# Kernel tuning notes

Measured on AMD Instinct MI355X. Metric: run time of the kernel, lower is better.

## Reference

```python
import jax, jax.numpy as jnp
import numpy as np
from jax import lax

A_SCALES = np.array([8., 16., 32.])
A_RATIOS = np.array([0.5, 1., 2.])
STRIDE = 16
PRE_NMS = 6000
POST_NMS = 300
NMS_THRESH = 0.7
MIN_SIZE = 16.0
NEG = -1e9


def _gen_anchors(base_size=16):
    w = h = float(base_size)
    x = y = 0.5 * (base_size - 1)
    size = w * h
    ws = np.round(np.sqrt(size / A_RATIOS))
    hs = np.round(ws * A_RATIOS)
    out = []
    for wi, hi in zip(ws, hs):
        WS = wi * A_SCALES
        HS = hi * A_SCALES
        out.append(np.stack([x - 0.5 * (WS - 1), y - 0.5 * (HS - 1),
                             x + 0.5 * (WS - 1), y + 0.5 * (HS - 1)], 1))
    return np.concatenate(out, 0).astype(np.float32)  # [9,4]

ANCHORS = _gen_anchors()


def _conv(x, w, b, pad):
    y = lax.conv_general_dilated(x, w, (1, 1), [(pad, pad), (pad, pad)],
                                 dimension_numbers=('NCHW', 'OIHW', 'NCHW'))
    return y + b[None, :, None, None]


def _nms(boxes, scores):
    # fixed-size greedy NMS: POST_NMS iterations of argmax + suppress
    areas = (boxes[:, 2] - boxes[:, 0] + 1.) * (boxes[:, 3] - boxes[:, 1] + 1.)
    def step(s, _):
        i = jnp.argmax(s)
        b = boxes[i]
        ix1 = jnp.maximum(b[0], boxes[:, 0]); iy1 = jnp.maximum(b[1], boxes[:, 1])
        ix2 = jnp.minimum(b[2], boxes[:, 2]); iy2 = jnp.minimum(b[3], boxes[:, 3])
        inter = jnp.maximum(ix2 - ix1 + 1., 0.) * jnp.maximum(iy2 - iy1 + 1., 0.)
        iou = inter / (areas[i] + areas - inter)
        return jnp.where(iou > NMS_THRESH, NEG, s), i
    _, keep = lax.scan(step, scores, None, length=POST_NMS)
    return keep


def reference(base_feat, img_info, gt_boxes, W1, b1, Wc, bc, Wb, bb):
    A = ANCHORS.shape[0]  # 9
    h = jax.nn.relu(_conv(base_feat, W1, b1, 1))          # [1,512,H,W]
    scores = _conv(h, Wc, bc, 0)                           # [1,2A,H,W]
    deltas = _conv(h, Wb, bb, 0)                           # [1,4A,H,W]
    H, W = scores.shape[2], scores.shape[3]
    # reshape(2) -> softmax over dim1 -> reshape back (RPN.reshape trick)
    probs = jax.nn.softmax(scores.reshape(1, 2, A * H, W), axis=1).reshape(1, 2 * A, H, W)
    fg = jnp.transpose(probs[0, A:], (1, 2, 0)).reshape(-1)      # [H*W*A], (h,w,a) order
    d = jnp.transpose(deltas[0], (1, 2, 0)).reshape(-1, 4)       # [H*W*A,4]
    sx, sy = jnp.meshgrid(jnp.arange(W, dtype=jnp.float32) * STRIDE,
                          jnp.arange(H, dtype=jnp.float32) * STRIDE)
    shifts = jnp.stack([sx, sy, sx, sy], -1).reshape(-1, 4)      # [H*W,4]
    anch = (shifts[:, None, :] + jnp.asarray(ANCHORS)[None, :, :]).reshape(-1, 4)
    # bbox_transform_inv
    wdt = anch[:, 2] - anch[:, 0] + 1.
    hgt = anch[:, 3] - anch[:, 1] + 1.
    cx = anch[:, 0] + 0.5 * wdt
    cy = anch[:, 1] + 0.5 * hgt
    pcx = d[:, 0] * wdt + cx
    pcy = d[:, 1] * hgt + cy
    pw = jnp.exp(d[:, 2]) * wdt
    ph = jnp.exp(d[:, 3]) * hgt
    x1 = jnp.clip(pcx - 0.5 * pw, 0., img_info[1] - 1.)
    y1 = jnp.clip(pcy - 0.5 * ph, 0., img_info[0] - 1.)
    x2 = jnp.clip(pcx + 0.5 * pw, 0., img_info[1] - 1.)
    y2 = jnp.clip(pcy + 0.5 * ph, 0., img_info[0] - 1.)
    props = jnp.stack([x1, y1, x2, y2], 1)
    ms = MIN_SIZE * img_info[2]
    valid = ((x2 - x1 + 1.) >= ms) & ((y2 - y1 + 1.) >= ms)
    sc = jnp.where(valid, fg, NEG)
    top_sc, top_idx = lax.top_k(sc, PRE_NMS)
    top_boxes = props[top_idx]
    keep = _nms(top_boxes, top_sc)
    out = top_boxes[keep]                                  # [POST_NMS,4]
    return jnp.concatenate([jnp.zeros((POST_NMS, 1), out.dtype), out], 1)


def setup_inputs() -> dict:
    key = jax.random.key(0)
    ks = jax.random.split(key, 6)
    H, W, C = 64, 96, 1024
    base_feat = jax.random.normal(ks[0], (1, C, H, W), jnp.float32)
    img_info = jnp.array([H * 16., W * 16., 1.], jnp.float32)
    gt_boxes = jax.random.uniform(ks[1], (8, 6), jnp.float32) * 100.0
    W1 = jax.random.normal(ks[2], (512, C, 3, 3), jnp.float32) * np.float32(np.sqrt(2.0 / (C * 9)))
    b1 = jnp.zeros((512,), jnp.float32)
    Wc = jax.random.normal(ks[3], (18, 512, 1, 1), jnp.float32) * np.float32(1.0 / np.sqrt(512))
    bc = jnp.zeros((18,), jnp.float32)
    Wb = jax.random.normal(ks[4], (36, 512, 1, 1), jnp.float32) * np.float32(0.01 / np.sqrt(512))
    bb = jnp.zeros((36,), jnp.float32)
    return {"base_feat": base_feat, "img_info": img_info, "gt_boxes": gt_boxes,
            "W1": W1, "b1": b1, "Wc": Wc, "bc": bc, "Wb": Wb, "bb": bb}
```

## Files before the change

### kernel.cpp

```cpp
#include <hip/hip_runtime.h>
#include <math.h>

#define HH 64
#define WW 96
#define NPX (HH*WW)
#define CIN 1024
#define CMID 512
#define NA 9
#define NANCH (NPX*NA)
#define PRE_NMS 6000
#define POST_NMS 300
#define NEGV -1e9f
#define NBINS 16384
#define BUFCAP 8192
#define MASKW 94

#define PYS 66
#define PXS 98
#define NCB 32
#define SCL 2048.0f
#define INV_SCL (1.0f/2048.0f)

#define K2_CS 16
#define K2_CC (CMID/K2_CS)

typedef _Float16 f16x8 __attribute__((ext_vector_type(8)));
typedef float f32x4 __attribute__((ext_vector_type(4)));

__constant__ float c_anch[9][4] = {
    {-84.f, -40.f,  99.f,  55.f},
    {-176.f,-88.f, 191.f, 103.f},
    {-360.f,-184.f,375.f, 199.f},
    {-56.f, -56.f,  71.f,  71.f},
    {-120.f,-120.f,135.f, 135.f},
    {-248.f,-248.f,263.f, 263.f},
    {-36.f, -80.f,  51.f,  95.f},
    {-80.f,-168.f,  95.f, 183.f},
    {-168.f,-344.f,183.f, 359.f}
};

__device__ __forceinline__ unsigned int fkey(float f) {
    unsigned int b = __float_as_uint(f);
    return (b & 0x80000000u) ? ~b : (b | 0x80000000u);
}
__device__ __forceinline__ float fkey_inv(unsigned int k) {
    unsigned int b = (k & 0x80000000u) ? (k & 0x7fffffffu) : ~k;
    return __uint_as_float(b);
}
__device__ __forceinline__ int score_bin(float s) {
    if (!(s > 0.f)) return 0;
    int b = (int)(s * (float)NBINS);
    return b > NBINS - 1 ? NBINS - 1 : b;
}

__global__ __launch_bounds__(256) void prep_x(const float* __restrict__ x,
                                              _Float16* __restrict__ xh,
                                              _Float16* __restrict__ xl) {
    __shared__ float t[64][65];
    int tid = threadIdx.x;
    int c0 = blockIdx.x * 64;
    int p0 = blockIdx.y * 64;
    int g = tid >> 6, l = tid & 63;
#pragma unroll
    for (int k = 0; k < 16; k++) {
        int cl = g * 16 + k;
        t[cl][l] = x[(size_t)(c0 + cl) * NPX + p0 + l];
    }
    __syncthreads();
#pragma unroll
    for (int k = 0; k < 16; k++) {
        int pl = g * 16 + k;
        int p = p0 + pl;
        int y = p / WW, xc = p - y * WW;
        int c = c0 + l;
        float v = t[l][pl];
        _Float16 hv = (_Float16)v;
        _Float16 lv = (_Float16)((v - (float)hv) * SCL);
        size_t o = (((size_t)(c >> 5) * PYS + (y + 1)) * PXS + (xc + 1)) * 32 + (c & 31);
        xh[o] = hv;
        xl[o] = lv;
    }
}

__global__ __launch_bounds__(256) void prep_w(const float* __restrict__ w,
                                              _Float16* __restrict__ wh,
                                              _Float16* __restrict__ wl) {
    __shared__ _Float16 sh[CIN * 9];
    __shared__ _Float16 sl[CIN * 9];
    int tid = threadIdx.x;
    int oc = blockIdx.x;
    for (int i = tid; i < CIN * 9; i += 256) {
        float v = w[(size_t)oc * CIN * 9 + i];
        _Float16 hv = (_Float16)v;
        sh[i] = hv;
        sl[i] = (_Float16)((v - (float)hv) * SCL);
    }
    __syncthreads();
    for (int i = tid; i < CIN * 9; i += 256) {
        int tap = i >> 10;
        int c = i & 1023;
        size_t o = (((size_t)tap * NCB + (c >> 5)) * CMID + oc) * 32 + (c & 31);
        wh[o] = sh[c * 9 + tap];
        wl[o] = sl[c * 9 + tap];
    }
}

__global__ __launch_bounds__(256, 2) void conv3_mfma(const _Float16* __restrict__ xh,
                                                     const _Float16* __restrict__ xl,
                                                     const _Float16* __restrict__ wh,
                                                     const _Float16* __restrict__ wl,
                                                     const float* __restrict__ b1,
                                                     float* __restrict__ h) {
    __shared__ float4 red[4][2][64];
    int tid = threadIdx.x;
    int lane = tid & 63;
    int wv = tid >> 6;
    int sp = blockIdx.x;
    int ty0 = (sp / 6) * 4;
    int tx0 = (sp % 6) * 16;
    int oc0 = blockIdx.y * 32;

    int la = lane & 15;
    int kg = lane >> 4;

    f32x4 acch[4][2], accc[4][2];
#pragma unroll
    for (int m = 0; m < 4; m++)
#pragma unroll
        for (int n = 0; n < 2; n++) {
            acch[m][n] = (f32x4){0.f, 0.f, 0.f, 0.f};
            accc[m][n] = (f32x4){0.f, 0.f, 0.f, 0.f};
        }

    int cb0 = wv * (NCB / 4);
    for (int cbi = 0; cbi < NCB / 4; cbi++) {
        int cb = cb0 + cbi;
#pragma unroll
        for (int tap = 0; tap < 9; tap++) {
            const int ky = tap / 3, kx = tap % 3;
            f16x8 ah[4], al[4];
#pragma unroll
            for (int m = 0; m < 4; m++) {
                int aoff = ((cb * PYS + (ty0 + m + ky)) * PXS + (tx0 + kx + la)) * 32 + kg * 8;
                ah[m] = *(const f16x8*)(xh + aoff);
                al[m] = *(const f16x8*)(xl + aoff);
            }
#pragma unroll
            for (int n = 0; n < 2; n++) {
                int boff = ((tap * NCB + cb) * CMID + oc0 + n * 16 + la) * 32 + kg * 8;
                f16x8 bh = *(const f16x8*)(wh + boff);
                f16x8 bl = *(const f16x8*)(wl + boff);
#pragma unroll
                for (int m = 0; m < 4; m++) {
                    acch[m][n] = __builtin_amdgcn_mfma_f32_16x16x32_f16(ah[m], bh, acch[m][n], 0, 0, 0);
                    accc[m][n] = __builtin_amdgcn_mfma_f32_16x16x32_f16(al[m], bh, accc[m][n], 0, 0, 0);
                    accc[m][n] = __builtin_amdgcn_mfma_f32_16x16x32_f16(ah[m], bl, accc[m][n], 0, 0, 0);
                }
            }
        }
    }

#pragma unroll
    for (int m = 0; m < 4; m++) {
        __syncthreads();
#pragma unroll
        for (int n = 0; n < 2; n++) {
            f32x4 t = acch[m][n];
            f32x4 c = accc[m][n];
            float4 w4;
            w4.x = t[0] + c[0] * INV_SCL;
            w4.y = t[1] + c[1] * INV_SCL;
            w4.z = t[2] + c[2] * INV_SCL;
            w4.w = t[3] + c[3] * INV_SCL;
            red[wv][n][lane] = w4;
        }
        __syncthreads();
        if (tid < 128) {
            int n = tid >> 6, l = tid & 63;
            float4 s0 = red[0][n][l], s1 = red[1][n][l];
            float4 s2 = red[2][n][l], s3 = red[3][n][l];
            int oc = oc0 + n * 16 + (l & 15);
            float bs = b1[oc];
            float4 s;
            s.x = fmaxf(s0.x + s1.x + s2.x + s3.x + bs, 0.f);
            s.y = fmaxf(s0.y + s1.y + s2.y + s3.y + bs, 0.f);
            s.z = fmaxf(s0.z + s1.z + s2.z + s3.z + bs, 0.f);
            s.w = fmaxf(s0.w + s1.w + s2.w + s3.w + bs, 0.f);
            int y = ty0 + m;
            int px0 = tx0 + (l >> 4) * 4;
            *(float4*)&h[(size_t)oc * NPX + y * WW + px0] = s;
        }
    }
}

__global__ __launch_bounds__(256) void conv1x1_part(const float* __restrict__ h,
                                                    const float* __restrict__ wc,
                                                    const float* __restrict__ wb,
                                                    float* __restrict__ psum) {
    __shared__ float wT[K2_CC][56];
    int tid = threadIdx.x;
    int px = blockIdx.x * 256 + tid;
    int g = blockIdx.y;
    int cb = g * K2_CC;
    for (int i = tid; i < K2_CC * 54; i += 256) {
        int c = i / 54, o = i - c * 54;
        float wv = (o < 18) ? wc[o * CMID + cb + c] : wb[(o - 18) * CMID + cb + c];
        wT[c][o] = wv;
    }
    __syncthreads();
    float acc[54];
#pragma unroll
    for (int o = 0; o < 54; o++) acc[o] = 0.f;
    for (int c = 0; c < K2_CC; c++) {
        float hv = h[(size_t)(cb + c) * NPX + px];
#pragma unroll
        for (int o = 0; o < 54; o++) acc[o] += wT[c][o] * hv;
    }
    for (int o = 0; o < 54; o++)
        psum[((size_t)g * 54 + o) * NPX + px] = acc[o];
}

__global__ __launch_bounds__(256) void conv1x1_reduce(const float* __restrict__ psum,
                                                      const float* __restrict__ bc,
                                                      const float* __restrict__ bb,
                                                      float* __restrict__ sd) {
    int i = blockIdx.x * 256 + threadIdx.x;
    if (i >= 54 * NPX) return;
    int o = i / NPX;
    float s = (o < 18) ? bc[o] : bb[o - 18];
    for (int g = 0; g < K2_CS; g++) s += psum[(size_t)g * 54 * NPX + i];
    sd[i] = s;
}

__global__ __launch_bounds__(256) void proposals_k(const float* __restrict__ sd,
                                                   const float* __restrict__ info,
                                                   float* __restrict__ props,
                                                   float* __restrict__ scv,
                                                   unsigned int* __restrict__ hist) {
    int i = blockIdx.x * 256 + threadIdx.x;
    if (i >= NANCH) return;
    int a = i % NA;
    int p = i / NA;
    int hy = p / WW, wx = p - hy * WW;

    float s0 = sd[a * NPX + p], s1 = sd[(a + NA) * NPX + p];
    float m = fmaxf(s0, s1);
    float e0 = expf(s0 - m), e1 = expf(s1 - m);
    float fg = e1 / (e0 + e1);

    float d0 = sd[(18 + 4 * a + 0) * NPX + p];
    float d1 = sd[(18 + 4 * a + 1) * NPX + p];
    float d2 = sd[(18 + 4 * a + 2) * NPX + p];
    float d3 = sd[(18 + 4 * a + 3) * NPX + p];

    float sx = wx * 16.f, sy = hy * 16.f;
    float ax1 = c_anch[a][0] + sx, ay1 = c_anch[a][1] + sy;
    float ax2 = c_anch[a][2] + sx, ay2 = c_anch[a][3] + sy;
    float wdt = ax2 - ax1 + 1.f;
    float hgt = ay2 - ay1 + 1.f;
    float cx = ax1 + 0.5f * wdt;
    float cy = ay1 + 0.5f * hgt;
    float pcx = d0 * wdt + cx;
    float pcy = d1 * hgt + cy;
    float pw = expf(d2) * wdt;
    float ph = expf(d3) * hgt;

    float imh = info[0], imw = info[1], iscale = info[2];
    float x1 = fminf(fmaxf(pcx - 0.5f * pw, 0.f), imw - 1.f);
    float y1 = fminf(fmaxf(pcy - 0.5f * ph, 0.f), imh - 1.f);
    float x2 = fminf(fmaxf(pcx + 0.5f * pw, 0.f), imw - 1.f);
    float y2 = fminf(fmaxf(pcy + 0.5f * ph, 0.f), imh - 1.f);

    float ms = 16.f * iscale;
    bool valid = ((x2 - x1 + 1.f) >= ms) && ((y2 - y1 + 1.f) >= ms);
    float s = valid ? fg : NEGV;

    props[(size_t)i * 4 + 0] = x1;
    props[(size_t)i * 4 + 1] = y1;
    props[(size_t)i * 4 + 2] = x2;
    props[(size_t)i * 4 + 3] = y2;
    scv[i] = s;
    atomicAdd(&hist[score_bin(s)], 1u);
}

__global__ __launch_bounds__(1024) void scan_hist(const unsigned int* __restrict__ hist,
                                                  unsigned int* __restrict__ params) {
    __shared__ unsigned int psum[1024];
    int tid = threadIdx.x;
    unsigned int s = 0;
    for (int k = 0; k < 16; k++) s += hist[tid * 16 + k];
    psum[tid] = s;
    __syncthreads();
    if (tid == 0) {
        unsigned int run = 0;
        int B = 0;
        int t;
        for (t = 1023; t >= 0; t--) {
            if (run + psum[t] >= PRE_NMS) break;
            run += psum[t];
        }
        if (t >= 0) {
            unsigned int r2 = run;
            B = t * 16;
            for (int b = t * 16 + 15; b >= t * 16; b--) {
                r2 += hist[b];
                if (r2 >= PRE_NMS) { B = b; break; }
            }
        }
        params[0] = (unsigned int)B;
    }
}

__global__ __launch_bounds__(256) void gather_top(const float* __restrict__ scv,
                                                  const unsigned int* __restrict__ params,
                                                  unsigned long long* __restrict__ buf,
                                                  unsigned int* __restrict__ counter) {
    int i = blockIdx.x * 256 + threadIdx.x;
    if (i >= NANCH) return;
    float s = scv[i];
    if (score_bin(s) >= (int)params[0]) {
        unsigned int pos = atomicAdd(counter, 1u);
        if (pos < BUFCAP) {
            unsigned long long key = ((unsigned long long)fkey(s) << 32) |
                                     (unsigned int)(~(unsigned int)i);
            buf[pos] = key;
        }
    }
}

__global__ __launch_bounds__(1024) void sort_top(unsigned long long* __restrict__ buf,
                                                 const unsigned int* __restrict__ counter,
                                                 const float* __restrict__ props,
                                                 float* __restrict__ top_boxes,
                                                 float* __restrict__ top_sc) {
    __shared__ unsigned long long arr[BUFCAP];
    int tid = threadIdx.x;
    unsigned int m = counter[0];
    if (m > BUFCAP) m = BUFCAP;
    for (int i = tid; i < BUFCAP; i += 1024) arr[i] = (i < (int)m) ? buf[i] : 0ULL;
    __syncthreads();
    for (int k = 2; k <= BUFCAP; k <<= 1) {
        for (int j = k >> 1; j > 0; j >>= 1) {
            for (int i = tid; i < BUFCAP; i += 1024) {
                int l = i ^ j;
                if (l > i) {
                    unsigned long long a = arr[i], b = arr[l];
                    bool dir = ((i & k) == 0);
                    if (dir ? (a < b) : (a > b)) { arr[i] = b; arr[l] = a; }
                }
            }
            __syncthreads();
        }
    }
    for (int t = tid; t < PRE_NMS; t += 1024) {
        unsigned long long v = arr[t];
        unsigned int key = (unsigned int)(v >> 32);
        unsigned int idx = ~((unsigned int)v);
        top_sc[t] = fkey_inv(key);
        float4 bx = *(const float4*)&props[(size_t)idx * 4];
        *(float4*)&top_boxes[(size_t)t * 4] = bx;
    }
}

__global__ __launch_bounds__(256) void iou_mask(const float* __restrict__ top_boxes,
                                                unsigned long long* __restrict__ mask) {
    int wid = (blockIdx.x * 256 + threadIdx.x) >> 6;
    int lane = threadIdx.x & 63;
    if (wid >= PRE_NMS) return;
    float4 b = *(const float4*)&top_boxes[(size_t)wid * 4];
    float ab = (b.z - b.x + 1.f) * (b.w - b.y + 1.f);
    for (int cj = 0; cj < MASKW; cj++) {
        int j = cj * 64 + lane;
        bool sup = false;
        if (j < PRE_NMS) {
            float4 c = *(const float4*)&top_boxes[(size_t)j * 4];
            float ac = (c.z - c.x + 1.f) * (c.w - c.y + 1.f);
            float ix1 = fmaxf(b.x, c.x), iy1 = fmaxf(b.y, c.y);
            float ix2 = fminf(b.z, c.z), iy2 = fminf(b.w, c.w);
            float inter = fmaxf(ix2 - ix1 + 1.f, 0.f) * fmaxf(iy2 - iy1 + 1.f, 0.f);
            float iou = inter / (ab + ac - inter);
            sup = iou > 0.7f;
        }
        unsigned long long m = __ballot(sup);
        if (lane == 0) mask[(size_t)wid * MASKW + cj] = m;
    }
}

__global__ __launch_bounds__(64) void nms_greedy(const float* __restrict__ top_boxes,
                                                 const unsigned long long* __restrict__ mask,
                                                 float* __restrict__ out) {
    int lane = threadIdx.x;
    unsigned long long r0 = 0ULL;
    unsigned long long r1;
    if (lane < 29)      r1 = 0ULL;
    else if (lane == 29) r1 = ~((1ULL << 48) - 1);
    else                r1 = ~0ULL;
    for (int t = 0; t < POST_NMS; t++) {
        unsigned long long w0 = ~r0;
        unsigned long long w1 = ~r1;
        unsigned long long B0 = __ballot(w0 != 0ULL);
        unsigned long long B1 = __ballot(w1 != 0ULL);
        int pos = 0;
        if (B0) {
            int wl = __builtin_ctzll(B0);
            unsigned long long bits = __shfl(w0, wl);
            pos = wl * 64 + __builtin_ctzll(bits);
        } else if (B1) {
            int wl = __builtin_ctzll(B1);
            unsigned long long bits = __shfl(w1, wl);
            pos = (64 + wl) * 64 + __builtin_ctzll(bits);
        }
        if (lane == 0) {
            float4 bb = *(const float4*)&top_boxes[(size_t)pos * 4];
            out[t * 5 + 0] = 0.f;
            out[t * 5 + 1] = bb.x;
            out[t * 5 + 2] = bb.y;
            out[t * 5 + 3] = bb.z;
            out[t * 5 + 4] = bb.w;
        }
        r0 |= mask[(size_t)pos * MASKW + lane];
        if (lane < 30) r1 |= mask[(size_t)pos * MASKW + 64 + lane];
    }
}

extern "C" void kernel_launch(void* const* d_in, const int* in_sizes, int n_in,
                              void* d_out, int out_size, void* d_ws, size_t ws_size,
                              hipStream_t stream) {
    const float* base = (const float*)d_in[0];
    const float* info = (const float*)d_in[1];
    const float* W1 = (const float*)d_in[3];
    const float* b1 = (const float*)d_in[4];
    const float* Wc = (const float*)d_in[5];
    const float* bc = (const float*)d_in[6];
    const float* Wb = (const float*)d_in[7];
    const float* Bb = (const float*)d_in[8];
    float* out = (float*)d_out;
    char* ws = (char*)d_ws;

    const size_t SZ_XT = (size_t)PYS * PXS * CIN * 2;
    const size_t SZ_WT = (size_t)9 * CMID * CIN * 2;
    const size_t OFF_XH = 0;
    const size_t OFF_XL = OFF_XH + SZ_XT;
    const size_t OFF_WH = OFF_XL + SZ_XT;
    const size_t OFF_WL = OFF_WH + SZ_WT;
    const size_t OFF_H  = OFF_WL + SZ_WT;
    const size_t OFF_SD   = OFF_H + (size_t)CMID * NPX * 4;
    const size_t OFF_PROPS= OFF_SD + (size_t)54 * NPX * 4;
    const size_t OFF_SCV  = OFF_PROPS + (size_t)NANCH * 16;
    const size_t OFF_HIST = OFF_SCV + (size_t)NANCH * 4;
    const size_t OFF_PAR  = OFF_HIST + (size_t)NBINS * 4;
    const size_t OFF_BUF  = OFF_PAR + 256;
    const size_t OFF_TB   = OFF_BUF + (size_t)BUFCAP * 8;
    const size_t OFF_TS   = OFF_TB + (size_t)PRE_NMS * 16;
    const size_t OFF_PSUM = OFF_XH;
    const size_t OFF_MASK = OFF_XH;

    _Float16* xh = (_Float16*)(ws + OFF_XH);
    _Float16* xl = (_Float16*)(ws + OFF_XL);
    _Float16* wh = (_Float16*)(ws + OFF_WH);
    _Float16* wl = (_Float16*)(ws + OFF_WL);
    float* h  = (float*)(ws + OFF_H);
    float* psum = (float*)(ws + OFF_PSUM);
    unsigned long long* mask = (unsigned long long*)(ws + OFF_MASK);
    float* sd = (float*)(ws + OFF_SD);
    float* props = (float*)(ws + OFF_PROPS);
    float* scv = (float*)(ws + OFF_SCV);
    unsigned int* hist = (unsigned int*)(ws + OFF_HIST);
    unsigned int* params = (unsigned int*)(ws + OFF_PAR);
    unsigned int* counter = params + 1;
    unsigned long long* buf = (unsigned long long*)(ws + OFF_BUF);
    float* top_boxes = (float*)(ws + OFF_TB);
    float* top_sc = (float*)(ws + OFF_TS);

    hipMemsetAsync(xh, 0, SZ_XT * 2, stream);
    hipMemsetAsync(hist, 0, (size_t)NBINS * 4 + 256, stream);

    prep_x<<<dim3(CIN / 64, NPX / 64), 256, 0, stream>>>(base, xh, xl);
    prep_w<<<CMID, 256, 0, stream>>>(W1, wh, wl);
    conv3_mfma<<<dim3(96, 16), 256, 0, stream>>>(xh, xl, wh, wl, b1, h);
    conv1x1_part<<<dim3(NPX / 256, K2_CS), 256, 0, stream>>>(h, Wc, Wb, psum);
    conv1x1_reduce<<<(54 * NPX) / 256, 256, 0, stream>>>(psum, bc, Bb, sd);
    proposals_k<<<NANCH / 256, 256, 0, stream>>>(sd, info, props, scv, hist);
    scan_hist<<<1, 1024, 0, stream>>>(hist, params);
    gather_top<<<NANCH / 256, 256, 0, stream>>>(scv, params, buf, counter);
    sort_top<<<1, 1024, 0, stream>>>(buf, counter, props, top_boxes, top_sc);
    iou_mask<<<(PRE_NMS * 64 + 255) / 256, 256, 0, stream>>>(top_boxes, mask);
    nms_greedy<<<1, 64, 0, stream>>>(top_boxes, mask, out);
}
```

Measured before the change: 648.4 us.

## Fuse prep kernels, reuse input rows across ky taps, raise conv occupancy

The two preprocessing kernels are merged into one launch, with the block index picking either the input transpose/split or the weight split. The 3x3 conv loop now loads six input rows once per kx and reuses them across the three ky taps, cutting redundant global loads. Launch bounds move from 2 to 3 blocks per CU to raise occupancy, and the 1x1 conv channel split drops from 16 to 4. The higher occupancy target may force register spills, since the larger A-fragment arrays add register pressure.

```diff
diff --git a/kernel.cpp b/kernel.cpp
--- a/kernel.cpp
+++ b/kernel.cpp
@@ -21,7 +21,7 @@
 #define SCL 2048.0f
 #define INV_SCL (1.0f/2048.0f)
 
-#define K2_CS 16
+#define K2_CS 4
 #define K2_CC (CMID/K2_CS)
 
 typedef _Float16 f16x8 __attribute__((ext_vector_type(8)));
@@ -53,59 +53,61 @@
     return b > NBINS - 1 ? NBINS - 1 : b;
 }
 
-__global__ __launch_bounds__(256) void prep_x(const float* __restrict__ x,
-                                              _Float16* __restrict__ xh,
-                                              _Float16* __restrict__ xl) {
-    __shared__ float t[64][65];
+__global__ __launch_bounds__(256) void prep_all(const float* __restrict__ x,
+                                                const float* __restrict__ w,
+                                                _Float16* __restrict__ xh,
+                                                _Float16* __restrict__ xl,
+                                                _Float16* __restrict__ wh,
+                                                _Float16* __restrict__ wl) {
+    __shared__ char smem[36864];
     int tid = threadIdx.x;
-    int c0 = blockIdx.x * 64;
-    int p0 = blockIdx.y * 64;
-    int g = tid >> 6, l = tid & 63;
-#pragma unroll
-    for (int k = 0; k < 16; k++) {
-        int cl = g * 16 + k;
-        t[cl][l] = x[(size_t)(c0 + cl) * NPX + p0 + l];
-    }
-    __syncthreads();
-#pragma unroll
-    for (int k = 0; k < 16; k++) {
-        int pl = g * 16 + k;
-        int p = p0 + pl;
-        int y = p / WW, xc = p - y * WW;
-        int c = c0 + l;
-        float v = t[l][pl];
-        _Float16 hv = (_Float16)v;
-        _Float16 lv = (_Float16)((v - (float)hv) * SCL);
-        size_t o = (((size_t)(c >> 5) * PYS + (y + 1)) * PXS + (xc + 1)) * 32 + (c & 31);
-        xh[o] = hv;
-        xl[o] = lv;
-    }
-}
-
-__global__ __launch_bounds__(256) void prep_w(const float* __restrict__ w,
-                                              _Float16* __restrict__ wh,
-                                              _Float16* __restrict__ wl) {
-    __shared__ _Float16 sh[CIN * 9];
-    __shared__ _Float16 sl[CIN * 9];
-    int tid = threadIdx.x;
-    int oc = blockIdx.x;
-    for (int i = tid; i < CIN * 9; i += 256) {
-        float v = w[(size_t)oc * CIN * 9 + i];
-        _Float16 hv = (_Float16)v;
-        sh[i] = hv;
-        sl[i] = (_Float16)((v - (float)hv) * SCL);
-    }
-    __syncthreads();
-    for (int i = tid; i < CIN * 9; i += 256) {
-        int tap = i >> 10;
-        int c = i & 1023;
-        size_t o = (((size_t)tap * NCB + (c >> 5)) * CMID + oc) * 32 + (c & 31);
-        wh[o] = sh[c * 9 + tap];
-        wl[o] = sl[c * 9 + tap];
-    }
-}
-
-__global__ __launch_bounds__(256, 2) void conv3_mfma(const _Float16* __restrict__ xh,
+    int bid = blockIdx.x;
+    if (bid < 1536) {
+        float (*t)[65] = (float(*)[65])smem;
+        int c0 = (bid & 15) * 64;
+        int p0 = (bid >> 4) * 64;
+        int g = tid >> 6, l = tid & 63;
+#pragma unroll
+        for (int k = 0; k < 16; k++) {
+            int cl = g * 16 + k;
+            t[cl][l] = x[(size_t)(c0 + cl) * NPX + p0 + l];
+        }
+        __syncthreads();
+#pragma unroll
+        for (int k = 0; k < 16; k++) {
+            int pl = g * 16 + k;
+            int p = p0 + pl;
+            int y = p / WW, xc = p - y * WW;
+            int c = c0 + l;
+            float v = t[l][pl];
+            _Float16 hv = (_Float16)v;
+            _Float16 lv = (_Float16)((v - (float)hv) * SCL);
+            size_t o = (((size_t)(c >> 5) * PYS + (y + 1)) * PXS + (xc + 1)) * 32 + (c & 31);
+            xh[o] = hv;
+            xl[o] = lv;
+        }
+    } else {
+        _Float16* sh = (_Float16*)smem;
+        _Float16* sl = (_Float16*)(smem + 18432);
+        int oc = bid - 1536;
+        for (int i = tid; i < CIN * 9; i += 256) {
+            float v = w[(size_t)oc * CIN * 9 + i];
+            _Float16 hv = (_Float16)v;
+            sh[i] = hv;
+            sl[i] = (_Float16)((v - (float)hv) * SCL);
+        }
+        __syncthreads();
+        for (int i = tid; i < CIN * 9; i += 256) {
+            int tap = i >> 10;
+            int c = i & 1023;
+            size_t o = (((size_t)tap * NCB + (c >> 5)) * CMID + oc) * 32 + (c & 31);
+            wh[o] = sh[c * 9 + tap];
+            wl[o] = sl[c * 9 + tap];
+        }
+    }
+}
+
+__global__ __launch_bounds__(256, 3) void conv3_mfma(const _Float16* __restrict__ xh,
                                                      const _Float16* __restrict__ xl,
                                                      const _Float16* __restrict__ wh,
                                                      const _Float16* __restrict__ wl,
@@ -136,25 +138,28 @@
     for (int cbi = 0; cbi < NCB / 4; cbi++) {
         int cb = cb0 + cbi;
 #pragma unroll
-        for (int tap = 0; tap < 9; tap++) {
-            const int ky = tap / 3, kx = tap % 3;
-            f16x8 ah[4], al[4];
-#pragma unroll
-            for (int m = 0; m < 4; m++) {
-                int aoff = ((cb * PYS + (ty0 + m + ky)) * PXS + (tx0 + kx + la)) * 32 + kg * 8;
-                ah[m] = *(const f16x8*)(xh + aoff);
-                al[m] = *(const f16x8*)(xl + aoff);
+        for (int kx = 0; kx < 3; kx++) {
+            f16x8 a6h[6], a6l[6];
+#pragma unroll
+            for (int r = 0; r < 6; r++) {
+                int aoff = ((cb * PYS + (ty0 + r)) * PXS + (tx0 + kx + la)) * 32 + kg * 8;
+                a6h[r] = *(const f16x8*)(xh + aoff);
+                a6l[r] = *(const f16x8*)(xl + aoff);
             }
 #pragma unroll
-            for (int n = 0; n < 2; n++) {
-                int boff = ((tap * NCB + cb) * CMID + oc0 + n * 16 + la) * 32 + kg * 8;
-                f16x8 bh = *(const f16x8*)(wh + boff);
-                f16x8 bl = *(const f16x8*)(wl + boff);
-#pragma unroll
-                for (int m = 0; m < 4; m++) {
-                    acch[m][n] = __builtin_amdgcn_mfma_f32_16x16x32_f16(ah[m], bh, acch[m][n], 0, 0, 0);
-                    accc[m][n] = __builtin_amdgcn_mfma_f32_16x16x32_f16(al[m], bh, accc[m][n], 0, 0, 0);
-                    accc[m][n] = __builtin_amdgcn_mfma_f32_16x16x32_f16(ah[m], bl, accc[m][n], 0, 0, 0);
+            for (int ky = 0; ky < 3; ky++) {
+                const int tap = ky * 3 + kx;
+#pragma unroll
+                for (int n = 0; n < 2; n++) {
+                    int boff = ((tap * NCB + cb) * CMID + oc0 + n * 16 + la) * 32 + kg * 8;
+                    f16x8 bh = *(const f16x8*)(wh + boff);
+                    f16x8 bl = *(const f16x8*)(wl + boff);
+#pragma unroll
+                    for (int m = 0; m < 4; m++) {
+                        acch[m][n] = __builtin_amdgcn_mfma_f32_16x16x32_f16(a6h[m + ky], bh, acch[m][n], 0, 0, 0);
+                        accc[m][n] = __builtin_amdgcn_mfma_f32_16x16x32_f16(a6l[m + ky], bh, accc[m][n], 0, 0, 0);
+                        accc[m][n] = __builtin_amdgcn_mfma_f32_16x16x32_f16(a6h[m + ky], bl, accc[m][n], 0, 0, 0);
+                    }
                 }
             }
         }
@@ -475,11 +480,10 @@
     hipMemsetAsync(xh, 0, SZ_XT * 2, stream);
     hipMemsetAsync(hist, 0, (size_t)NBINS * 4 + 256, stream);
 
-    prep_x<<<dim3(CIN / 64, NPX / 64), 256, 0, stream>>>(base, xh, xl);
-    prep_w<<<CMID, 256, 0, stream>>>(W1, wh, wl);
+    prep_all<<<2048, 256, 0, stream>>>(base, W1, xh, xl, wh, wl);
     conv3_mfma<<<dim3(96, 16), 256, 0, stream>>>(xh, xl, wh, wl, b1, h);
     conv1x1_part<<<dim3(NPX / 256, K2_CS), 256, 0, stream>>>(h, Wc, Wb, psum);
-    conv1x1_reduce<<<(54 * NPX) / 256, 256, 0, stream>>>(psum, bc, Bb, sd);
+    conv1x1_reduce<<<(54 * NPX + 255) / 256, 256, 0, stream>>>(psum, bc, Bb, sd);
     proposals_k<<<NANCH / 256, 256, 0, stream>>>(sd, info, props, scv, hist);
     scan_hist<<<1, 1024, 0, stream>>>(hist, params);
     gather_top<<<NANCH / 256, 256, 0, stream>>>(scv, params, buf, counter);
```

Result: no change. 637.0 us (-1.8%).

## Reuse conv input rows across ky taps, raise occupancy, triangular IoU mask

Applied to the files above, without the earlier changes.

The 3x3 conv kernel now loads six input rows once per kx and reuses them for all three ky taps, instead of reloading four rows per tap. Launch bounds go from 2 to 3 waves per SIMD to raise occupancy, which limits registers and may cause spills given the larger live A fragments. The IoU mask kernel skips work below the diagonal (j < i) and writes zero words there, which assumes greedy NMS only reads suppression of later boxes. The conv1x1_reduce grid size is also rounded up.

```diff
diff --git a/kernel.cpp b/kernel.cpp
--- a/kernel.cpp
+++ b/kernel.cpp
@@ -105,7 +105,7 @@
     }
 }
 
-__global__ __launch_bounds__(256, 2) void conv3_mfma(const _Float16* __restrict__ xh,
+__global__ __launch_bounds__(256, 3) void conv3_mfma(const _Float16* __restrict__ xh,
                                                      const _Float16* __restrict__ xl,
                                                      const _Float16* __restrict__ wh,
                                                      const _Float16* __restrict__ wl,
@@ -136,25 +136,28 @@
     for (int cbi = 0; cbi < NCB / 4; cbi++) {
         int cb = cb0 + cbi;
 #pragma unroll
-        for (int tap = 0; tap < 9; tap++) {
-            const int ky = tap / 3, kx = tap % 3;
-            f16x8 ah[4], al[4];
-#pragma unroll
-            for (int m = 0; m < 4; m++) {
-                int aoff = ((cb * PYS + (ty0 + m + ky)) * PXS + (tx0 + kx + la)) * 32 + kg * 8;
-                ah[m] = *(const f16x8*)(xh + aoff);
-                al[m] = *(const f16x8*)(xl + aoff);
+        for (int kx = 0; kx < 3; kx++) {
+            f16x8 a6h[6], a6l[6];
+#pragma unroll
+            for (int r = 0; r < 6; r++) {
+                int aoff = ((cb * PYS + (ty0 + r)) * PXS + (tx0 + kx + la)) * 32 + kg * 8;
+                a6h[r] = *(const f16x8*)(xh + aoff);
+                a6l[r] = *(const f16x8*)(xl + aoff);
             }
 #pragma unroll
-            for (int n = 0; n < 2; n++) {
-                int boff = ((tap * NCB + cb) * CMID + oc0 + n * 16 + la) * 32 + kg * 8;
-                f16x8 bh = *(const f16x8*)(wh + boff);
-                f16x8 bl = *(const f16x8*)(wl + boff);
-#pragma unroll
-                for (int m = 0; m < 4; m++) {
-                    acch[m][n] = __builtin_amdgcn_mfma_f32_16x16x32_f16(ah[m], bh, acch[m][n], 0, 0, 0);
-                    accc[m][n] = __builtin_amdgcn_mfma_f32_16x16x32_f16(al[m], bh, accc[m][n], 0, 0, 0);
-                    accc[m][n] = __builtin_amdgcn_mfma_f32_16x16x32_f16(ah[m], bl, accc[m][n], 0, 0, 0);
+            for (int ky = 0; ky < 3; ky++) {
+                const int tap = ky * 3 + kx;
+#pragma unroll
+                for (int n = 0; n < 2; n++) {
+                    int boff = ((tap * NCB + cb) * CMID + oc0 + n * 16 + la) * 32 + kg * 8;
+                    f16x8 bh = *(const f16x8*)(wh + boff);
+                    f16x8 bl = *(const f16x8*)(wl + boff);
+#pragma unroll
+                    for (int m = 0; m < 4; m++) {
+                        acch[m][n] = __builtin_amdgcn_mfma_f32_16x16x32_f16(a6h[m + ky], bh, acch[m][n], 0, 0, 0);
+                        accc[m][n] = __builtin_amdgcn_mfma_f32_16x16x32_f16(a6l[m + ky], bh, accc[m][n], 0, 0, 0);
+                        accc[m][n] = __builtin_amdgcn_mfma_f32_16x16x32_f16(a6h[m + ky], bl, accc[m][n], 0, 0, 0);
+                    }
                 }
             }
         }
@@ -370,18 +373,21 @@
     float4 b = *(const float4*)&top_boxes[(size_t)wid * 4];
     float ab = (b.z - b.x + 1.f) * (b.w - b.y + 1.f);
     for (int cj = 0; cj < MASKW; cj++) {
-        int j = cj * 64 + lane;
-        bool sup = false;
-        if (j < PRE_NMS) {
-            float4 c = *(const float4*)&top_boxes[(size_t)j * 4];
-            float ac = (c.z - c.x + 1.f) * (c.w - c.y + 1.f);
-            float ix1 = fmaxf(b.x, c.x), iy1 = fmaxf(b.y, c.y);
-            float ix2 = fminf(b.z, c.z), iy2 = fminf(b.w, c.w);
-            float inter = fmaxf(ix2 - ix1 + 1.f, 0.f) * fmaxf(iy2 - iy1 + 1.f, 0.f);
-            float iou = inter / (ab + ac - inter);
-            sup = iou > 0.7f;
-        }
-        unsigned long long m = __ballot(sup);
+        unsigned long long m = 0ULL;
+        if ((cj + 1) * 64 > wid) {
+            int j = cj * 64 + lane;
+            bool sup = false;
+            if (j < PRE_NMS && j >= wid) {
+                float4 c = *(const float4*)&top_boxes[(size_t)j * 4];
+                float ac = (c.z - c.x + 1.f) * (c.w - c.y + 1.f);
+                float ix1 = fmaxf(b.x, c.x), iy1 = fmaxf(b.y, c.y);
+                float ix2 = fminf(b.z, c.z), iy2 = fminf(b.w, c.w);
+                float inter = fmaxf(ix2 - ix1 + 1.f, 0.f) * fmaxf(iy2 - iy1 + 1.f, 0.f);
+                float iou = inter / (ab + ac - inter);
+                sup = iou > 0.7f;
+            }
+            m = __ballot(sup);
+        }
         if (lane == 0) mask[(size_t)wid * MASKW + cj] = m;
     }
 }
@@ -479,7 +485,7 @@
     prep_w<<<CMID, 256, 0, stream>>>(W1, wh, wl);
     conv3_mfma<<<dim3(96, 16), 256, 0, stream>>>(xh, xl, wh, wl, b1, h);
     conv1x1_part<<<dim3(NPX / 256, K2_CS), 256, 0, stream>>>(h, Wc, Wb, psum);
-    conv1x1_reduce<<<(54 * NPX) / 256, 256, 0, stream>>>(psum, bc, Bb, sd);
+    conv1x1_reduce<<<(54 * NPX + 255) / 256, 256, 0, stream>>>(psum, bc, Bb, sd);
     proposals_k<<<NANCH / 256, 256, 0, stream>>>(sd, info, props, scv, hist);
     scan_hist<<<1, 1024, 0, stream>>>(hist, params);
     gather_top<<<NANCH / 256, 256, 0, stream>>>(scv, params, buf, counter);
```

New measurement: 611.7 us. 5.7% less time.
